# Optimization experiments

Measured on AMD Instinct MI355X. Metric: run time of the kernel, lower is better.

The kernel has to match this reference:

```python
import jax, jax.numpy as jnp
import numpy as np

N = 100000
EPS = 1e-5
NEG_SLOPE = 0.2


def gat_conv(x, src, dst, W, a_src, a_dst, b):
    # x: [N, din]; W: [dout, din]; a_src/a_dst/b: [dout]
    h = x @ W.T                              # [N, dout]
    alpha_s = h @ a_src                      # [N]
    alpha_d = h @ a_dst                      # [N]
    e = jax.nn.leaky_relu(alpha_s[src] + alpha_d[dst], NEG_SLOPE)  # [E]
    # segment softmax over incoming edges of each destination node
    emax = jax.ops.segment_max(e, dst, num_segments=N)
    ex = jnp.exp(e - emax[dst])
    denom = jax.ops.segment_sum(ex, dst, num_segments=N)
    alpha = ex / denom[dst]                  # [E]
    out = jax.ops.segment_sum(alpha[:, None] * h[src], dst, num_segments=N)
    return out + b


def batch_norm(x, gamma, beta):
    mu = jnp.mean(x, axis=0)
    var = jnp.var(x, axis=0)
    return gamma * (x - mu) * jax.lax.rsqrt(var + EPS) + beta


def setup_inputs() -> dict:
    key = jax.random.key(0)
    ks = jax.random.split(key, 20)
    din, dh, dout = 128, 128, 128
    E = 1600000
    x = jax.random.normal(ks[0], (N, din), dtype=jnp.float32)
    edge_index = jax.random.randint(ks[1], (2, E), 0, N, dtype=jnp.int32)
    def glorot(k, shape):
        fan = sum(shape)
        s = jnp.sqrt(6.0 / fan)
        return jax.random.uniform(k, shape, dtype=jnp.float32, minval=-s, maxval=s)
    inp = {"x": x, "edge_index": edge_index}
    dims = [(din, dh), (dh, dh), (dh, dout)]
    for l, (di, do) in enumerate(dims):
        inp[f"W{l}"] = glorot(ks[2 + 4 * l], (do, di))
        inp[f"a_src{l}"] = glorot(ks[3 + 4 * l], (do,)) * 0.1
        inp[f"a_dst{l}"] = glorot(ks[4 + 4 * l], (do,)) * 0.1
        inp[f"b{l}"] = jnp.zeros((do,), dtype=jnp.float32)
    for l in range(2):
        inp[f"gamma{l}"] = jnp.ones((dh,), dtype=jnp.float32)
        inp[f"beta{l}"] = jnp.zeros((dh,), dtype=jnp.float32)
    return inp


def reference(x, edge_index, W0, a_src0, a_dst0, b0, W1, a_src1, a_dst1, b1,
              W2, a_src2, a_dst2, b2, gamma0, beta0, gamma1, beta1):
    # add self-loops (PyG GATConv default)
    ar = jnp.arange(N, dtype=edge_index.dtype)
    src = jnp.concatenate([edge_index[0], ar])
    dst = jnp.concatenate([edge_index[1], ar])
    h = gat_conv(x, src, dst, W0, a_src0, a_dst0, b0)
    h = jax.nn.relu(batch_norm(h, gamma0, beta0))
    h = gat_conv(h, src, dst, W1, a_src1, a_dst1, b1)
    h = jax.nn.relu(batch_norm(h, gamma1, beta1))
    out = gat_conv(h, src, dst, W2, a_src2, a_dst2, b2)
    return out
```

## Files before the change

kernel.cpp:

```cpp
#include <hip/hip_runtime.h>
#include <cstdint>
#include <cstddef>

#define NN 100000
#define NP 100096
#define EE 1600000
#define ET 1700000
#define NBKT 196
#define TILE 2048
#define STAT_BLOCKS 400

typedef short  bf16x8 __attribute__((ext_vector_type(8)));
typedef float  f32x4  __attribute__((ext_vector_type(4)));

__device__ __forceinline__ unsigned short f2bf(float f) {
    unsigned int x = __builtin_bit_cast(unsigned int, f);
    x += 0x7FFFu + ((x >> 16) & 1u);
    return (unsigned short)(x >> 16);
}
__device__ __forceinline__ unsigned int pk2(float lo, float hi) {
    return ((unsigned int)f2bf(hi) << 16) | (unsigned int)f2bf(lo);
}
__device__ __forceinline__ float bflo(unsigned int u) {
    return __builtin_bit_cast(float, u << 16);
}
__device__ __forceinline__ float bfhi(unsigned int u) {
    return __builtin_bit_cast(float, u & 0xFFFF0000u);
}


__global__ void k_bcount(const int* __restrict__ ei, int* __restrict__ btot) {
    __shared__ int h[256];
    int t = threadIdx.x;
    h[t] = 0;
    __syncthreads();
    for (int e = blockIdx.x * 256 + t; e < ET; e += 256 * 256) {
        int d = (e < EE) ? ei[EE + e] : (e - EE);
        atomicAdd(&h[d >> 9], 1);
    }
    __syncthreads();
    if (h[t]) atomicAdd(&btot[t], h[t]);
}

__global__ void k_bscan(const int* __restrict__ btot, int* __restrict__ bstart,
                        int* __restrict__ bcur, int* __restrict__ off) {
    __shared__ int s[256];
    int t = threadIdx.x;
    int v = (t < NBKT) ? btot[t] : 0;
    s[t] = v;
    __syncthreads();
    for (int o = 1; o < 256; o <<= 1) {
        int a = (t >= o) ? s[t - o] : 0;
        __syncthreads();
        s[t] += a;
        __syncthreads();
    }
    int ex = s[t] - v;
    if (t <= NBKT) bstart[t] = (t < NBKT) ? ex : ET;
    if (t == NBKT - 1) bstart[NBKT] = s[t];
    bcur[t] = ex;
    if (t == 0) off[NN] = ET;
}

__global__ __launch_bounds__(256) void k_bucket(
    const int* __restrict__ ei, int* __restrict__ bcur, unsigned int* __restrict__ bucketed)
{
    __shared__ int h4[4][256], woff[4][256], loff[256], gbase[256], sc[256];
    __shared__ unsigned int stage[TILE];
    __shared__ int gaddr[TILE];
    __shared__ int stot_s;
    const int t = threadIdx.x;
    const int w = t >> 6;
    const int e0 = blockIdx.x * TILE;

    h4[0][t] = 0; h4[1][t] = 0; h4[2][t] = 0; h4[3][t] = 0;
    __syncthreads();

    unsigned int pk[TILE / 256];
    int bk[TILE / 256];
#pragma unroll
    for (int i = 0; i < TILE / 256; ++i) {
        int e = e0 + i * 256 + t;
        bk[i] = -1;
        if (e < ET) {
            int s, d;
            if (e < EE) { s = ei[e]; d = ei[EE + e]; } else { s = e - EE; d = s; }
            bk[i] = d >> 9;
            pk[i] = ((unsigned int)(d & 511) << 17) | (unsigned int)s;
            atomicAdd(&h4[w][bk[i]], 1);
        }
    }
    __syncthreads();

    int h0 = h4[0][t], h1 = h4[1][t], h2 = h4[2][t], h3 = h4[3][t];
    int tot = h0 + h1 + h2 + h3;
    sc[t] = tot;
    __syncthreads();
    for (int o = 1; o < 256; o <<= 1) {
        int a = (t >= o) ? sc[t - o] : 0;
        __syncthreads();
        sc[t] += a;
        __syncthreads();
    }
    int lo = sc[t] - tot;
    loff[t] = lo;
    woff[0][t] = lo;
    woff[1][t] = lo + h0;
    woff[2][t] = lo + h0 + h1;
    woff[3][t] = lo + h0 + h1 + h2;
    if (t < NBKT && tot) gbase[t] = atomicAdd(&bcur[t], tot);
    if (t == 255) stot_s = sc[255];
    h4[0][t] = 0; h4[1][t] = 0; h4[2][t] = 0; h4[3][t] = 0;
    __syncthreads();

#pragma unroll
    for (int i = 0; i < TILE / 256; ++i) {
        if (bk[i] >= 0) {
            int b = bk[i];
            int r = woff[w][b] + atomicAdd(&h4[w][b], 1);
            stage[r] = pk[i];
            gaddr[r] = gbase[b] + (r - loff[b]);
        }
    }
    __syncthreads();

    const int stot = stot_s;
    for (int j = t; j < stot; j += 256)
        bucketed[gaddr[j]] = stage[j];
}

__global__ __launch_bounds__(256) void k_csr(
    const unsigned int* __restrict__ bucketed, const int* __restrict__ bstart,
    int* __restrict__ off, int* __restrict__ srcs)
{
    __shared__ int h[512], sc2[512], c2[512], sp[256];
    const int t = threadIdx.x;
    const int b = blockIdx.x;
    const int beg = bstart[b], end = bstart[b + 1];
    const int cnt = end - beg;

    h[t] = 0; h[t + 256] = 0; c2[t] = 0; c2[t + 256] = 0;
    __syncthreads();
    for (int i = t; i < cnt; i += 256)
        atomicAdd(&h[bucketed[beg + i] >> 17], 1);
    __syncthreads();

    int a0 = h[2 * t], a1 = h[2 * t + 1];
    sp[t] = a0 + a1;
    __syncthreads();
    for (int o = 1; o < 256; o <<= 1) {
        int a = (t >= o) ? sp[t - o] : 0;
        __syncthreads();
        sp[t] += a;
        __syncthreads();
    }
    int ep = sp[t] - (a0 + a1);
    sc2[2 * t] = ep;
    sc2[2 * t + 1] = ep + a0;
    __syncthreads();

    const int d0 = b << 9;
#pragma unroll
    for (int k = t; k < 512; k += 256) {
        int d = d0 + k;
        if (d < NN) off[d] = beg + sc2[k];
    }

    for (int i = t; i < cnt; i += 256) {
        unsigned int v = bucketed[beg + i];
        int ld = v >> 17;
        int r = atomicAdd(&c2[ld], 1);
        srcs[beg + sc2[ld] + r] = (int)(v & 0x1FFFFu);
    }
}

__global__ void k_cvtw3(const float* __restrict__ W0, const float* __restrict__ W1,
                        const float* __restrict__ W2, unsigned short* __restrict__ Wb) {
    int i = blockIdx.x * 256 + threadIdx.x;
    const float* W = (i < 16384) ? W0 : (i < 32768) ? W1 : W2;
    Wb[i] = f2bf(W[i & 16383]);
}

template<int MODE>
__global__ __launch_bounds__(256) void k_mfma(
    const void* __restrict__ Xv, const unsigned short* __restrict__ Wb,
    const float* __restrict__ gsum, const float* __restrict__ gsq,
    const float* __restrict__ gamma, const float* __restrict__ beta,
    const float* __restrict__ asrc, const float* __restrict__ adst,
    unsigned short* __restrict__ Hb, float* __restrict__ AS, float* __restrict__ AD)
{
    __shared__ float hst[4][16][132];
    __shared__ float scale_s[128], shift_s[128];
    const int t    = threadIdx.x;
    const int w    = t >> 6;
    const int lane = t & 63;
    const int c    = lane & 15;
    const int q    = lane >> 4;
    const int r0   = blockIdx.x * 64 + w * 16;
    const int row  = r0 + c;

    if (MODE) {
        if (t < 128) {
            float mu  = gsum[t] * (1.f / NN);
            float var = gsq[t] * (1.f / NN) - mu * mu;
            float sc  = gamma[t] * rsqrtf(var + 1e-5f);
            scale_s[t] = sc;
            shift_s[t] = beta[t] - mu * sc;
        }
        __syncthreads();
    }

    union { uint4 u; bf16x8 v; } Af[4];
    if (row < NN) {
        if (MODE) {
            const unsigned short* xp = (const unsigned short*)Xv + ((size_t)row << 7) + (q << 3);
#pragma unroll
            for (int k0 = 0; k0 < 4; ++k0) {
                uint4 r = *(const uint4*)(xp + (k0 << 5));
                const int kb = (k0 << 5) + (q << 3);
                float a0 = bflo(r.x), a1 = bfhi(r.x), a2 = bflo(r.y), a3 = bfhi(r.y);
                float a4 = bflo(r.z), a5 = bfhi(r.z), a6 = bflo(r.w), a7 = bfhi(r.w);
                float4 sA = *(const float4*)&scale_s[kb];
                float4 sB = *(const float4*)&scale_s[kb + 4];
                float4 hA = *(const float4*)&shift_s[kb];
                float4 hB = *(const float4*)&shift_s[kb + 4];
                a0 = fmaxf(0.f, fmaf(a0, sA.x, hA.x));
                a1 = fmaxf(0.f, fmaf(a1, sA.y, hA.y));
                a2 = fmaxf(0.f, fmaf(a2, sA.z, hA.z));
                a3 = fmaxf(0.f, fmaf(a3, sA.w, hA.w));
                a4 = fmaxf(0.f, fmaf(a4, sB.x, hB.x));
                a5 = fmaxf(0.f, fmaf(a5, sB.y, hB.y));
                a6 = fmaxf(0.f, fmaf(a6, sB.z, hB.z));
                a7 = fmaxf(0.f, fmaf(a7, sB.w, hB.w));
                Af[k0].u.x = pk2(a0, a1);
                Af[k0].u.y = pk2(a2, a3);
                Af[k0].u.z = pk2(a4, a5);
                Af[k0].u.w = pk2(a6, a7);
            }
        } else {
            const float* xp = (const float*)Xv + ((size_t)row << 7) + (q << 3);
#pragma unroll
            for (int k0 = 0; k0 < 4; ++k0) {
                float4 a = *(const float4*)(xp + (k0 << 5));
                float4 b = *(const float4*)(xp + (k0 << 5) + 4);
                Af[k0].u.x = pk2(a.x, a.y);
                Af[k0].u.y = pk2(a.z, a.w);
                Af[k0].u.z = pk2(b.x, b.y);
                Af[k0].u.w = pk2(b.z, b.w);
            }
        }
    } else {
#pragma unroll
        for (int k0 = 0; k0 < 4; ++k0) Af[k0].u = make_uint4(0, 0, 0, 0);
    }

    f32x4 acc[8];
#pragma unroll
    for (int nt = 0; nt < 8; ++nt) acc[nt] = (f32x4){0.f, 0.f, 0.f, 0.f};

#pragma unroll
    for (int nt = 0; nt < 8; ++nt) {
        union { uint4 u; bf16x8 v; } Bf[4];
        const size_t bbase = ((size_t)(nt * 16 + c) << 7) + (q << 3);
#pragma unroll
        for (int k0 = 0; k0 < 4; ++k0)
            Bf[k0].u = *(const uint4*)(Wb + bbase + (k0 << 5));
#pragma unroll
        for (int k0 = 0; k0 < 4; ++k0)
            acc[nt] = __builtin_amdgcn_mfma_f32_16x16x32_bf16(Af[k0].v, Bf[k0].v, acc[nt], 0, 0, 0);
    }

    float ps[4] = {0.f, 0.f, 0.f, 0.f}, pd[4] = {0.f, 0.f, 0.f, 0.f};
#pragma unroll
    for (int nt = 0; nt < 8; ++nt) {
        float av = asrc[nt * 16 + c];
        float dv = adst[nt * 16 + c];
#pragma unroll
        for (int r = 0; r < 4; ++r) {
            ps[r] = fmaf(acc[nt][r], av, ps[r]);
            pd[r] = fmaf(acc[nt][r], dv, pd[r]);
        }
    }
#pragma unroll
    for (int m = 1; m < 16; m <<= 1) {
#pragma unroll
        for (int r = 0; r < 4; ++r) { ps[r] += __shfl_xor(ps[r], m); pd[r] += __shfl_xor(pd[r], m); }
    }
    if (c == 0) {
#pragma unroll
        for (int r = 0; r < 4; ++r) {
            int grow = r0 + q * 4 + r;
            if (grow < NN) { AS[grow] = ps[r]; AD[grow] = pd[r]; }
        }
    }

#pragma unroll
    for (int nt = 0; nt < 8; ++nt)
#pragma unroll
        for (int r = 0; r < 4; ++r)
            hst[w][q * 4 + r][nt * 16 + c] = acc[nt][r];
    __syncthreads();
    {
        const int orow = lane >> 2, seg = lane & 3;
        const int grow = r0 + orow;
        if (grow < NN) {
#pragma unroll
            for (int i = 0; i < 4; ++i) {
                float4 a = *(const float4*)&hst[w][orow][seg * 32 + i * 8];
                float4 b = *(const float4*)&hst[w][orow][seg * 32 + i * 8 + 4];
                uint4 o;
                o.x = pk2(a.x, a.y); o.y = pk2(a.z, a.w);
                o.z = pk2(b.x, b.y); o.w = pk2(b.z, b.w);
                *(uint4*)(Hb + ((size_t)grow << 7) + seg * 32 + i * 8) = o;
            }
        }
    }
}

template<int OUTBF>
__global__ __launch_bounds__(256) void k_agg(
    const int* __restrict__ off, const int* __restrict__ srcs,
    const unsigned short* __restrict__ Hb, const float* __restrict__ AS,
    const float* __restrict__ AD, const float* __restrict__ bias,
    void* __restrict__ OUT)
{
    __shared__ uint2 s_e[4][64];
    const int wid  = threadIdx.x >> 6;
    const int lane = threadIdx.x & 63;
    const int g    = lane >> 4;
    const int x16  = lane & 15;
    const int n    = blockIdx.x * 4 + wid;
    const int beg = off[n], end = off[n + 1];
    const float adn = AD[n];

    float acc[8];
#pragma unroll
    for (int i = 0; i < 8; ++i) acc[i] = 0.f;
    float den = 0.f;

    for (int base = beg; base < end; base += 64) {
        int cnt = end - base; if (cnt > 64) cnt = 64;
        float wgt = 0.f; int s = 0;
        if (lane < cnt) {
            s = srcs[base + lane];
            float e = AS[s] + adn;
            e = (e > 0.f) ? e : 0.2f * e;
            wgt = __expf(e);
        }
        s_e[wid][lane] = make_uint2((unsigned int)s, __builtin_bit_cast(unsigned int, wgt));
        den += wgt;
        int rounds = (cnt + 3) >> 2;
        for (int j = 0; j < rounds; ++j) {
            uint2 ew = s_e[wid][(j << 2) + g];
            float wq = __builtin_bit_cast(float, ew.y);
            uint4 u = *((const uint4*)(Hb + ((size_t)ew.x << 7)) + x16);
            acc[0] = fmaf(wq, bflo(u.x), acc[0]);
            acc[1] = fmaf(wq, bfhi(u.x), acc[1]);
            acc[2] = fmaf(wq, bflo(u.y), acc[2]);
            acc[3] = fmaf(wq, bfhi(u.y), acc[3]);
            acc[4] = fmaf(wq, bflo(u.z), acc[4]);
            acc[5] = fmaf(wq, bfhi(u.z), acc[5]);
            acc[6] = fmaf(wq, bflo(u.w), acc[6]);
            acc[7] = fmaf(wq, bfhi(u.w), acc[7]);
        }
    }

#pragma unroll
    for (int i = 0; i < 8; ++i) {
        acc[i] += __shfl_xor(acc[i], 16);
        acc[i] += __shfl_xor(acc[i], 32);
    }
#pragma unroll
    for (int o = 32; o; o >>= 1) den += __shfl_xor(den, o);
    float inv = 1.f / den;

    if (g == 0) {
        float4 b1 = *(const float4*)&bias[x16 << 3];
        float4 b2 = *(const float4*)&bias[(x16 << 3) + 4];
        float o0 = fmaf(acc[0], inv, b1.x), o1 = fmaf(acc[1], inv, b1.y);
        float o2 = fmaf(acc[2], inv, b1.z), o3 = fmaf(acc[3], inv, b1.w);
        float o4 = fmaf(acc[4], inv, b2.x), o5 = fmaf(acc[5], inv, b2.y);
        float o6 = fmaf(acc[6], inv, b2.z), o7 = fmaf(acc[7], inv, b2.w);
        if (OUTBF) {
            uint4 pkd;
            pkd.x = pk2(o0, o1); pkd.y = pk2(o2, o3);
            pkd.z = pk2(o4, o5); pkd.w = pk2(o6, o7);
            *(uint4*)((unsigned short*)OUT + ((size_t)n << 7) + (x16 << 3)) = pkd;
        } else {
            float* op = (float*)OUT + ((size_t)n << 7) + (x16 << 3);
            *(float4*)op = make_float4(o0, o1, o2, o3);
            *(float4*)(op + 4) = make_float4(o4, o5, o6, o7);
        }
    }
}

__global__ __launch_bounds__(256) void k_colsum(const unsigned int* __restrict__ Xb,
                                                float* __restrict__ gsum, float* __restrict__ gsq) {
    __shared__ float ls[4][128], lq[4][128];
    const int t = threadIdx.x;
    const int c2 = t & 63;
    const int half = t >> 6;
    float s0 = 0.f, s1 = 0.f, q0 = 0.f, q1 = 0.f;
    for (int r = blockIdx.x * 4 + half; r < NN; r += STAT_BLOCKS * 4) {
        unsigned int v = Xb[(size_t)r * 64 + c2];
        float f0 = bflo(v), f1 = bfhi(v);
        s0 += f0; q0 += f0 * f0;
        s1 += f1; q1 += f1 * f1;
    }
    ls[half][2 * c2] = s0; ls[half][2 * c2 + 1] = s1;
    lq[half][2 * c2] = q0; lq[half][2 * c2 + 1] = q1;
    __syncthreads();
    if (t < 128) {
        float ss = ls[0][t] + ls[1][t] + ls[2][t] + ls[3][t];
        float qq = lq[0][t] + lq[1][t] + lq[2][t] + lq[3][t];
        atomicAdd(&gsum[t], ss);
        atomicAdd(&gsq[t], qq);
    }
}

extern "C" void kernel_launch(void* const* d_in, const int* in_sizes, int n_in,
                              void* d_out, int out_size, void* d_ws, size_t ws_size,
                              hipStream_t stream)
{
    const float* x  = (const float*)d_in[0];
    const int*   ei = (const int*)d_in[1];
    const float* Wm[3]  = {(const float*)d_in[2], (const float*)d_in[6],  (const float*)d_in[10]};
    const float* Asr[3] = {(const float*)d_in[3], (const float*)d_in[7],  (const float*)d_in[11]};
    const float* Ads[3] = {(const float*)d_in[4], (const float*)d_in[8],  (const float*)d_in[12]};
    const float* Bs[3]  = {(const float*)d_in[5], (const float*)d_in[9],  (const float*)d_in[13]};
    const float* gam[2] = {(const float*)d_in[14], (const float*)d_in[16]};
    const float* bet[2] = {(const float*)d_in[15], (const float*)d_in[17]};

    char* p = (char*)d_ws;
    auto carve = [&](size_t bytes) -> char* {
        char* r = p;
        p += (bytes + 255) & ~(size_t)255;
        return r;
    };
    int*   off_   = (int*)carve((size_t)(NN + 1) * 4);
    int*   srcs   = (int*)carve((size_t)ET * 4);
    unsigned int* bucketed = (unsigned int*)carve((size_t)ET * 4);
    int*   btot   = (int*)carve(256 * 4);
    float* gstat  = (float*)carve(4 * 128 * 4);
    int*   bstart = (int*)carve(260 * 4);
    int*   bcur   = (int*)carve(256 * 4);
    unsigned short* Hb  = (unsigned short*)carve((size_t)NP * 128 * 2);
    unsigned short* Wb  = (unsigned short*)carve((size_t)3 * 16384 * 2);
    float* AS    = (float*)carve((size_t)NN * 4);
    float* AD    = (float*)carve((size_t)NN * 4);

    float*          OUTf = (float*)d_out;
    unsigned short* OUTb = (unsigned short*)d_out;

    (void)hipMemsetAsync(btot, 0, 256 * 4 + 4 * 128 * 4, stream);

    k_bcount<<<256, 256, 0, stream>>>(ei, btot);
    k_bscan<<<1, 256, 0, stream>>>(btot, bstart, bcur, off_);
    k_bucket<<<(ET + TILE - 1) / TILE, 256, 0, stream>>>(ei, bcur, bucketed);
    k_csr<<<NBKT, 256, 0, stream>>>(bucketed, bstart, off_, srcs);

    k_cvtw3<<<192, 256, 0, stream>>>(Wm[0], Wm[1], Wm[2], Wb);

    const int MFMA_GRID = NP / 64;

    k_mfma<0><<<MFMA_GRID, 256, 0, stream>>>(x, Wb, nullptr, nullptr, nullptr, nullptr,
                                             Asr[0], Ads[0], Hb, AS, AD);
    k_agg<1><<<NN / 4, 256, 0, stream>>>(off_, srcs, Hb, AS, AD, Bs[0], OUTb);
    k_colsum<<<STAT_BLOCKS, 256, 0, stream>>>((const unsigned int*)OUTb, gstat, gstat + 128);

    k_mfma<1><<<MFMA_GRID, 256, 0, stream>>>(OUTb, Wb + 16384, gstat, gstat + 128,
                                             gam[0], bet[0], Asr[1], Ads[1], Hb, AS, AD);
    k_agg<1><<<NN / 4, 256, 0, stream>>>(off_, srcs, Hb, AS, AD, Bs[1], OUTb);
    k_colsum<<<STAT_BLOCKS, 256, 0, stream>>>((const unsigned int*)OUTb, gstat + 256, gstat + 384);

    k_mfma<1><<<MFMA_GRID, 256, 0, stream>>>(OUTb, Wb + 32768, gstat + 256, gstat + 384,
                                             gam[1], bet[1], Asr[2], Ads[2], Hb, AS, AD);
    k_agg<0><<<NN / 4, 256, 0, stream>>>(off_, srcs, Hb, AS, AD, Bs[2], OUTf);
}
```

Measured before the change: 562.4 us.

## Store hidden features in permuted column order to skip LDS transpose

The MFMA kernel now writes each lane's accumulator columns directly as packed bf16 in an interleaved (permuted) column order, which removes the shared-memory staging buffer and the extra barrier. Downstream consumers are adjusted to match: the weights of the next layers have their input columns permuted, BN gamma/beta are read through the inverse permutation, and the aggregation kernel reads the bias and writes the final fp32 output with strided indexing to restore natural order. This removes LDS traffic and a sync, but the final fp32 stores become 4-byte scattered writes instead of float4 vector stores.

```diff
diff --git a/kernel.cpp b/kernel.cpp
--- a/kernel.cpp
+++ b/kernel.cpp
@@ -27,6 +27,7 @@
 __device__ __forceinline__ float bfhi(unsigned int u) {
     return __builtin_bit_cast(float, u & 0xFFFF0000u);
 }
+__device__ __forceinline__ int unperm(int j) { return ((j & 7) << 4) | (j >> 3); }
 
 
 __global__ void k_bcount(const int* __restrict__ ei, int* __restrict__ btot) {
@@ -177,8 +178,11 @@
 __global__ void k_cvtw3(const float* __restrict__ W0, const float* __restrict__ W1,
                         const float* __restrict__ W2, unsigned short* __restrict__ Wb) {
     int i = blockIdx.x * 256 + threadIdx.x;
-    const float* W = (i < 16384) ? W0 : (i < 32768) ? W1 : W2;
-    Wb[i] = f2bf(W[i & 16383]);
+    int layer = i >> 14;
+    const float* W = (layer == 0) ? W0 : (layer == 1) ? W1 : W2;
+    int base = i & 16383;
+    int src = (layer == 0) ? base : ((base & ~127) | unperm(base & 127));
+    Wb[i] = f2bf(W[src]);
 }
 
 template<int MODE>
@@ -189,23 +193,22 @@
     const float* __restrict__ asrc, const float* __restrict__ adst,
     unsigned short* __restrict__ Hb, float* __restrict__ AS, float* __restrict__ AD)
 {
-    __shared__ float hst[4][16][132];
     __shared__ float scale_s[128], shift_s[128];
     const int t    = threadIdx.x;
-    const int w    = t >> 6;
     const int lane = t & 63;
     const int c    = lane & 15;
     const int q    = lane >> 4;
-    const int r0   = blockIdx.x * 64 + w * 16;
+    const int r0   = blockIdx.x * 64 + (t >> 6) * 16;
     const int row  = r0 + c;
 
     if (MODE) {
         if (t < 128) {
+            int ot = unperm(t);
             float mu  = gsum[t] * (1.f / NN);
             float var = gsq[t] * (1.f / NN) - mu * mu;
-            float sc  = gamma[t] * rsqrtf(var + 1e-5f);
+            float sc  = gamma[ot] * rsqrtf(var + 1e-5f);
             scale_s[t] = sc;
-            shift_s[t] = beta[t] - mu * sc;
+            shift_s[t] = beta[ot] - mu * sc;
         }
         __syncthreads();
     }
@@ -295,24 +298,15 @@
     }
 
 #pragma unroll
-    for (int nt = 0; nt < 8; ++nt)
-#pragma unroll
-        for (int r = 0; r < 4; ++r)
-            hst[w][q * 4 + r][nt * 16 + c] = acc[nt][r];
-    __syncthreads();
-    {
-        const int orow = lane >> 2, seg = lane & 3;
-        const int grow = r0 + orow;
+    for (int r = 0; r < 4; ++r) {
+        int grow = r0 + q * 4 + r;
         if (grow < NN) {
-#pragma unroll
-            for (int i = 0; i < 4; ++i) {
-                float4 a = *(const float4*)&hst[w][orow][seg * 32 + i * 8];
-                float4 b = *(const float4*)&hst[w][orow][seg * 32 + i * 8 + 4];
-                uint4 o;
-                o.x = pk2(a.x, a.y); o.y = pk2(a.z, a.w);
-                o.z = pk2(b.x, b.y); o.w = pk2(b.z, b.w);
-                *(uint4*)(Hb + ((size_t)grow << 7) + seg * 32 + i * 8) = o;
-            }
+            uint4 o;
+            o.x = pk2(acc[0][r], acc[1][r]);
+            o.y = pk2(acc[2][r], acc[3][r]);
+            o.z = pk2(acc[4][r], acc[5][r]);
+            o.w = pk2(acc[6][r], acc[7][r]);
+            *(uint4*)(Hb + ((size_t)grow << 7) + (c << 3)) = o;
         }
     }
 }
@@ -375,21 +369,20 @@
     float inv = 1.f / den;
 
     if (g == 0) {
-        float4 b1 = *(const float4*)&bias[x16 << 3];
-        float4 b2 = *(const float4*)&bias[(x16 << 3) + 4];
-        float o0 = fmaf(acc[0], inv, b1.x), o1 = fmaf(acc[1], inv, b1.y);
-        float o2 = fmaf(acc[2], inv, b1.z), o3 = fmaf(acc[3], inv, b1.w);
-        float o4 = fmaf(acc[4], inv, b2.x), o5 = fmaf(acc[5], inv, b2.y);
-        float o6 = fmaf(acc[6], inv, b2.z), o7 = fmaf(acc[7], inv, b2.w);
+        float o8[8];
+#pragma unroll
+        for (int i = 0; i < 8; ++i)
+            o8[i] = fmaf(acc[i], inv, bias[i * 16 + x16]);
         if (OUTBF) {
             uint4 pkd;
-            pkd.x = pk2(o0, o1); pkd.y = pk2(o2, o3);
-            pkd.z = pk2(o4, o5); pkd.w = pk2(o6, o7);
+            pkd.x = pk2(o8[0], o8[1]); pkd.y = pk2(o8[2], o8[3]);
+            pkd.z = pk2(o8[4], o8[5]); pkd.w = pk2(o8[6], o8[7]);
             *(uint4*)((unsigned short*)OUT + ((size_t)n << 7) + (x16 << 3)) = pkd;
         } else {
-            float* op = (float*)OUT + ((size_t)n << 7) + (x16 << 3);
-            *(float4*)op = make_float4(o0, o1, o2, o3);
-            *(float4*)(op + 4) = make_float4(o4, o5, o6, o7);
+            float* op = (float*)OUT + ((size_t)n << 7) + x16;
+#pragma unroll
+            for (int i = 0; i < 8; ++i)
+                op[i * 16] = o8[i];
         }
     }
 }
```

After: 535.0 us. 1.05x faster.
